# Performance work log

Measured on AMD Instinct MI355X. Metric: run time of the kernel, lower is better.

The kernel has to match this reference:

```python
import jax, jax.numpy as jnp
import numpy as np

# ---- constants from vecpar / module globals ----
N_SAMPLE = 500000
HID = 64       # shared_layers = [64]
HEAD = 32      # q*_layers width
PERIOD = 30
KAPPA, Y_BAR, B, C = 0.2, 2.0, 1.0, 0.1
GAMMA, RHO, SIGMA, DT = 1.2, 0.03, 0.03, 0.005


def _glorot(key, shape):
    fan_in, fan_out = shape
    std = (2.0 / (fan_in + fan_out)) ** 0.5
    return std * jax.random.normal(key, shape, dtype=jnp.float32)


def setup_inputs() -> dict:
    key = jax.random.key(0)
    ks = jax.random.split(key, 8)
    Y = jax.random.uniform(ks[0], (N_SAMPLE, 2), minval=0.05, maxval=5.0, dtype=jnp.float32)
    z = lambda n: jnp.zeros((n,), dtype=jnp.float32)
    return {
        'Y': Y,
        'W0': _glorot(ks[1], (2, HID)),   'b0': z(HID),
        'Wh1': _glorot(ks[2], (HID, HEAD)), 'bh1': z(HEAD), 'Wo1': _glorot(ks[3], (HEAD, 1)), 'bo1': z(1),
        'Wh2': _glorot(ks[4], (HID, HEAD)), 'bh2': z(HEAD), 'Wo2': _glorot(ks[5], (HEAD, 1)), 'bo2': z(1),
        'Wh3': _glorot(ks[6], (HID, HEAD)), 'bh3': z(HEAD), 'Wo3': _glorot(ks[7], (HEAD, 1)), 'bo3': z(1),
    }


def _net(Y2, Y3, W0, b0, Wh1, bh1, Wo1, bo1, Wh2, bh2, Wo2, bo2, Wh3, bh3, Wo3, bo3):
    # shared trunk: concat -> Dense(64) -> tanh; heads: Dense(32)->tanh->Dense(1)->exp
    h = jnp.tanh(jnp.concatenate([Y2, Y3], axis=1) @ W0 + b0)
    q1 = jnp.exp(jnp.tanh(h @ Wh1 + bh1) @ Wo1 + bo1)
    q2 = jnp.exp(jnp.tanh(h @ Wh2 + bh2) @ Wo2 + bo2)
    q3 = jnp.exp(jnp.tanh(h @ Wh3 + bh3) @ Wo3 + bo3)
    return q1, q2, q3


def _forward(Y, W0, b0, Wh1, bh1, Wo1, bo1, Wh2, bh2, Wo2, bo2, Wh3, bh3, Wo3, bo3):
    params = (W0, b0, Wh1, bh1, Wo1, bo1, Wh2, bh2, Wo2, bo2, Wh3, bh3, Wo3, bo3)
    f = lambda y2, y3: _net(y2, y3, *params)

    def q_and_grads(y2, y3):
        # per-row scalar sensitivities via two jvp passes (equiv. to tape.gradient)
        ones = jnp.ones_like(y2); zeros = jnp.zeros_like(y2)
        (q1, q2, q3), (d12, d22, d32) = jax.jvp(f, (y2, y3), (ones, zeros))
        _, (d13, d23, d33) = jax.jvp(f, (y2, y3), (zeros, ones))
        s11 = d12 * SIGMA / q1; s21 = d22 * SIGMA / q2; s31 = d32 * SIGMA / q3
        s12 = d13 * SIGMA / q1; s22 = d23 * SIGMA / q2; s32 = d33 * SIGMA / q3
        return (q1, q2, q3), (s11, s21, s31, s12, s22, s32)

    n = Y.shape[0]
    Y2 = Y[:, :1]; Y3 = Y[:, 1:2]
    (q1, q2, q3), (s11, s21, s31, s12, s22, s32) = q_and_grads(Y2, Y3)

    # dZ already scaled by sqrt(dt)
    noise = jnp.sqrt(jnp.asarray(DT, Y.dtype)) * jax.random.normal(
        jax.random.key(42), (PERIOD, n, 1, 2), dtype=Y.dtype)

    def step(carry, dZ):
        q1, q2, q3, Y2, Y3, s11, s21, s31, s12, s22, s32, loss = carry
        dZ1 = dZ[..., 0]; dZ2 = dZ[..., 1]
        W = q1 + q2 + q3
        q1h = q1 / W; q2h = q2 / W; q3h = 1 - q1h - q2h
        c = B * q1 - C * q1 ** 2 + Y2 + Y3
        sc1 = B * q1 * s11 - 2 * C * q1 ** 2 * s11 + SIGMA
        sc2 = B * q1 * s12 - 2 * C * q1 ** 2 * s12 + SIGMA
        sW1 = q1 * s11 + q2 * s21 + q3 * s31
        sW2 = q1 * s12 + q2 * s22 + q3 * s32
        g = GAMMA / (GAMMA - 1)
        sJ1 = g * (sc1 / c - sW1 / W); sJ2 = g * (sc2 / c - sW2 / W)
        p1 = (GAMMA * q1h * (s11 ** 2 + s12 ** 2)
              + GAMMA * q2h * (s11 * s21 + s12 * s22)
              + GAMMA * q3h * (s11 * s31 + s12 * s32)
              - (1 - GAMMA) * (sJ1 * s11 + sJ2 * s12))
        p2 = (GAMMA * q1h * (s11 * s21 + s12 * s22)
              + GAMMA * q2h * (s21 ** 2 + s22 ** 2)
              + GAMMA * q3h * (s21 * s31 + s22 * s32)
              - (1 - GAMMA) * (sJ1 * s21 + sJ2 * s22))
        p3 = (GAMMA * q1h * (s11 * s31 + s12 * s32)
              + GAMMA * q2h * (s21 * s31 + s22 * s32)
              + GAMMA * q3h * (s31 ** 2 + s32 ** 2)
              - (1 - GAMMA) * (sJ1 * s31 + sJ2 * s32))
        muY2 = KAPPA * (Y_BAR - Y2); muY3 = KAPPA * (Y_BAR - Y3)
        r = (RHO
             + GAMMA * ((B * q1 - 2 * C * q1 ** 2) * (p1 - (B - C * q1))
                        - C * q1 ** 2 * (s11 ** 2 + s12 ** 2) + muY2 + muY3) / c
             - GAMMA * (GAMMA + 1) / 2 * (sc1 ** 2 + sc2 ** 2) / c ** 2)
        r = r / (1 - GAMMA * (B * q1 - 2 * C * q1 ** 2) / c)
        mu1 = r + p1 - (B - C * q1)
        mu2 = r + p2 - Y2 / q2
        mu3 = r + p3 - Y3 / q3
        q1n = q1 * (1 + mu1 * DT + s11 * dZ1 + s12 * dZ2)
        q2n = q2 * (1 + mu2 * DT + s21 * dZ1 + s22 * dZ2)
        q3n = q3 * (1 + mu3 * DT + s31 * dZ1 + s32 * dZ2)
        Y2n = Y2 + muY2 * DT + SIGMA * dZ1
        Y3n = Y3 + muY3 * DT + SIGMA * dZ2
        (q1t, q2t, q3t), (ns11, ns21, ns31, ns12, ns22, ns32) = q_and_grads(Y2n, Y3n)
        loss = loss + jnp.sum((q1n - q1t) ** 2 + (q2n - q2t) ** 2 + (q3n - q3t) ** 2) / (n * PERIOD)
        return (q1n, q2n, q3n, Y2n, Y3n, ns11, ns21, ns31, ns12, ns22, ns32, loss), None

    init = (q1, q2, q3, Y2, Y3, s11, s21, s31, s12, s22, s32, jnp.asarray(0.0, Y.dtype))
    carry, _ = jax.lax.scan(step, init, noise)
    return carry[-1]


def reference(Y, W0, b0, Wh1, bh1, Wo1, bo1, Wh2, bh2, Wo2, bo2, Wh3, bh3, Wo3, bo3):
    return _forward(Y, W0, b0, Wh1, bh1, Wo1, bo1, Wh2, bh2, Wo2, bo2, Wh3, bh3, Wo3, bo3)
```

## Files before the change

kernel.cpp:

```cpp
#include <hip/hip_runtime.h>
#include <hip/hip_bf16.h>
#include <stdint.h>

#define NB 256
#define PERIOD 30

typedef __bf16  bf16x8 __attribute__((ext_vector_type(8)));
typedef float   f32x4  __attribute__((ext_vector_type(4)));
typedef float   f32x2  __attribute__((ext_vector_type(2)));
typedef unsigned int uint4v __attribute__((ext_vector_type(4)));

__device__ __forceinline__ float frcp(float x){ return __builtin_amdgcn_rcpf(x); }

__device__ __forceinline__ float fast_tanh(float x){
  float e = __expf(2.0f*x);
  return fmaf(-2.0f, frcp(e + 1.0f), 1.0f);
}

__device__ __forceinline__ unsigned int f2bfbits(float x){
  union { __hip_bfloat16 b; unsigned short u; } v;
  v.b = __float2bfloat16(x);
  return (unsigned int)v.u;
}
__device__ __forceinline__ unsigned int pack2bf(float lo, float hi){
  return f2bfbits(lo) | (f2bfbits(hi) << 16);
}

template <int CTRL>
__device__ __forceinline__ float dpp_add_step(float x){
  int y = __builtin_amdgcn_update_dpp(0, __float_as_int(x), CTRL, 0xf, 0xf, true);
  return x + __int_as_float(y);
}
__device__ __forceinline__ float row16_sum(float x){
  x = dpp_add_step<0xB1>(x);
  x = dpp_add_step<0x4E>(x);
  x = dpp_add_step<0x124>(x);
  x = dpp_add_step<0x128>(x);
  return x;
}

__device__ __forceinline__ void threefry2x32_k42(uint32_t x0, uint32_t x1,
                                                 uint32_t& o0, uint32_t& o1){
  const uint32_t ks0 = 0u, ks1 = 42u, ks2 = 0u ^ 42u ^ 0x1BD11BDAu;
  x0 += ks0; x1 += ks1;
#define TFR(rot) { x0 += x1; x1 = (x1 << (rot)) | (x1 >> (32 - (rot))); x1 ^= x0; }
  TFR(13) TFR(15) TFR(26) TFR(6)
  x0 += ks1; x1 += ks2 + 1u;
  TFR(17) TFR(29) TFR(16) TFR(24)
  x0 += ks2; x1 += ks0 + 2u;
  TFR(13) TFR(15) TFR(26) TFR(6)
  x0 += ks0; x1 += ks1 + 3u;
  TFR(17) TFR(29) TFR(16) TFR(24)
  x0 += ks1; x1 += ks2 + 4u;
  TFR(13) TFR(15) TFR(26) TFR(6)
  x0 += ks2; x1 += ks0 + 5u;
#undef TFR
  o0 = x0; o1 = x1;
}

__device__ __forceinline__ float normal_from_bits(uint32_t bits){
  float f = __uint_as_float((bits >> 9) | 0x3f800000u) - 1.0f;
  const float lo = -0.99999994f;
  float u = fmaf(f, 2.0f, lo);
  u = fmaxf(u, lo);
  float w = -log1pf(-u*u);
  float p;
  if (w < 5.0f){
    float ww = w - 2.5f;
    p = 2.81022636e-08f;
    p = fmaf(p, ww, 3.43273939e-07f);
    p = fmaf(p, ww, -3.5233877e-06f);
    p = fmaf(p, ww, -4.39150654e-06f);
    p = fmaf(p, ww, 0.00021858087f);
    p = fmaf(p, ww, -0.00125372503f);
    p = fmaf(p, ww, -0.00417768164f);
    p = fmaf(p, ww, 0.246640727f);
    p = fmaf(p, ww, 1.50140941f);
  } else {
    float ww = sqrtf(w) - 3.0f;
    p = -0.000200214257f;
    p = fmaf(p, ww, 0.000100950558f);
    p = fmaf(p, ww, 0.00134934322f);
    p = fmaf(p, ww, -0.00367342844f);
    p = fmaf(p, ww, 0.00573950773f);
    p = fmaf(p, ww, -0.0076224613f);
    p = fmaf(p, ww, 0.00943887047f);
    p = fmaf(p, ww, 1.00167406f);
    p = fmaf(p, ww, 2.83297682f);
  }
  return 1.41421356f * (p * u);
}

__device__ __forceinline__ void stage_tile(char* buf, int st, int grp, int colL,
    const unsigned int* hp, const unsigned int* up){
  if (grp == st){
    const int rbase = colL * 128;
    const int sw = (colL & 7) << 4;
#pragma unroll
    for (int w = 0; w < 8; ++w){
      int off = rbase + ((w * 16) ^ sw);
      *(uint4v*)(buf + off)        = uint4v{hp[w*4], hp[w*4+1], hp[w*4+2], hp[w*4+3]};
      *(uint4v*)(buf + 2048 + off) = uint4v{up[w*4], up[w*4+1], up[w*4+2], up[w*4+3]};
    }
  }
}

__device__ __forceinline__ void net_eval(
    float y2, float y3,
    const float* __restrict__ W0, const float* __restrict__ b0,
    char* sAw,
    const char* __restrict__ sBb,
    int colL, int grp,
    const float (&bh_v)[3][2], const float (&wo_v)[3][2], const float* bo_v,
    float& q1o, float& q2o, float& q3o,
    float& s11, float& s21, float& s31,
    float& s12, float& s22, float& s32)
{
  unsigned int hp[32], up[32];
#pragma unroll
  for (int d = 0; d < 32; ++d){
    f32x2 w0a = *(const f32x2*)(W0 + 2*d);
    f32x2 w0b = *(const f32x2*)(W0 + 64 + 2*d);
    f32x2 b0v = *(const f32x2*)(b0 + 2*d);
    f32x2 pre = y2 * w0a + (y3 * w0b + b0v);
    float hA = fast_tanh(pre.x), hB = fast_tanh(pre.y);
    f32x2 h  = {hA, hB};
    f32x2 u  = 1.0f - h * h;
    hp[d] = pack2bf(hA, hB);
    up[d] = pack2bf(u.x, u.y);
  }

  float qraw[3] = {0,0,0}, Araw[3] = {0,0,0}, Braw[3] = {0,0,0};
  const int bsw  = (colL & 7) << 4;
  const int srcL = ((colL >> 2) << 4) | colL;

#pragma unroll 1
  for (int st = 0; st < 4; ++st){
    stage_tile(sAw, st, grp, colL, hp, up);

    bf16x8 afh[2], afu[2];
#pragma unroll
    for (int kt = 0; kt < 2; ++kt){
      int off = colL*128 + ((kt*64 + grp*16) ^ bsw);
      afh[kt] = *(const bf16x8*)(sAw + off);
      afu[kt] = *(const bf16x8*)(sAw + 2048 + off);
    }

#pragma unroll
    for (int hd = 0; hd < 3; ++hd){
      f32x2 aq01 = {0,0}, aq23 = {0,0};
      f32x2 aA01 = {0,0}, aA23 = {0,0};
      f32x2 aB01 = {0,0}, aB23 = {0,0};
#pragma unroll
      for (int nt = 0; nt < 2; ++nt){
        bf16x8 bW[2], bA[2], bB[2];
#pragma unroll
        for (int kt = 0; kt < 2; ++kt){
          int rbase2 = (hd*96 + nt*16 + colL) * 128;
          int ko = ((kt*64 + grp*16) ^ bsw);
          bW[kt] = *(const bf16x8*)(sBb + rbase2 + ko);
          bA[kt] = *(const bf16x8*)(sBb + rbase2 + 4096 + ko);
          bB[kt] = *(const bf16x8*)(sBb + rbase2 + 8192 + ko);
        }
        f32x4 cAT = {0,0,0,0}, cA2 = {0,0,0,0}, cA3 = {0,0,0,0};
#pragma unroll
        for (int kt = 0; kt < 2; ++kt){
          cAT = __builtin_amdgcn_mfma_f32_16x16x32_bf16(afh[kt], bW[kt], cAT, 0, 0, 0);
          cA2 = __builtin_amdgcn_mfma_f32_16x16x32_bf16(afu[kt], bA[kt], cA2, 0, 0, 0);
          cA3 = __builtin_amdgcn_mfma_f32_16x16x32_bf16(afu[kt], bB[kt], cA3, 0, 0, 0);
        }
        float bh = bh_v[hd][nt], wo = wo_v[hd][nt];
        float t0 = fast_tanh(cAT[0] + bh);
        float t1 = fast_tanh(cAT[1] + bh);
        float t2 = fast_tanh(cAT[2] + bh);
        float t3 = fast_tanh(cAT[3] + bh);
        f32x2 dt01 = {fmaf(-t0, t0, 1.0f), fmaf(-t1, t1, 1.0f)};
        f32x2 dt23 = {fmaf(-t2, t2, 1.0f), fmaf(-t3, t3, 1.0f)};
        f32x2 wo2 = {wo, wo};
        aq01 = aq01 + f32x2{t0, t1} * wo2;
        aq23 = aq23 + f32x2{t2, t3} * wo2;
        aA01 = aA01 + dt01 * f32x2{cA2[0], cA2[1]};
        aA23 = aA23 + dt23 * f32x2{cA2[2], cA2[3]};
        aB01 = aB01 + dt01 * f32x2{cA3[0], cA3[1]};
        aB23 = aB23 + dt23 * f32x2{cA3[2], cA3[3]};
      }
      float rq0 = row16_sum(aq01.x), rq1 = row16_sum(aq01.y);
      float rq2 = row16_sum(aq23.x), rq3 = row16_sum(aq23.y);
      float rA0 = row16_sum(aA01.x), rA1 = row16_sum(aA01.y);
      float rA2 = row16_sum(aA23.x), rA3 = row16_sum(aA23.y);
      float rB0 = row16_sum(aB01.x), rB1 = row16_sum(aB01.y);
      float rB2 = row16_sum(aB23.x), rB3 = row16_sum(aB23.y);
      float qsel = (colL & 2) ? ((colL & 1) ? rq3 : rq2)
                              : ((colL & 1) ? rq1 : rq0);
      float asel = (colL & 2) ? ((colL & 1) ? rA3 : rA2)
                              : ((colL & 1) ? rA1 : rA0);
      float bsel = (colL & 2) ? ((colL & 1) ? rB3 : rB2)
                              : ((colL & 1) ? rB1 : rB0);
      float qp = __shfl(qsel, srcL, 64);
      float ap = __shfl(asel, srcL, 64);
      float bp = __shfl(bsel, srcL, 64);
      bool keep = (st == grp);
      qraw[hd] = keep ? qp : qraw[hd];
      Araw[hd] = keep ? ap : Araw[hd];
      Braw[hd] = keep ? bp : Braw[hd];
    }
  }

  q1o = __expf(qraw[0] + bo_v[0]);
  q2o = __expf(qraw[1] + bo_v[1]);
  q3o = __expf(qraw[2] + bo_v[2]);
  s11 = Araw[0]; s21 = Araw[1]; s31 = Araw[2];
  s12 = Braw[0]; s22 = Braw[1]; s32 = Braw[2];
}

__global__ __launch_bounds__(NB)
void sim_kernel(const float* __restrict__ Y,
  const float* __restrict__ W0,  const float* __restrict__ b0,
  const float* __restrict__ Wh1, const float* __restrict__ bh1,
  const float* __restrict__ Wo1, const float* __restrict__ bo1,
  const float* __restrict__ Wh2, const float* __restrict__ bh2,
  const float* __restrict__ Wo2, const float* __restrict__ bo2,
  const float* __restrict__ Wh3, const float* __restrict__ bh3,
  const float* __restrict__ Wo3, const float* __restrict__ bo3,
  float* __restrict__ out, int n)
{
  __shared__ __align__(16) char sB[288 * 128];
  __shared__ __align__(16) char sA[4][2 * 16 * 128];

  for (int e = threadIdx.x; e < 18432; e += NB){
    int hd   = e / 6144;
    int rem  = e - hd * 6144;
    int mat  = rem >> 11;
    int rem2 = rem & 2047;
    int j = rem2 >> 5, i = rem2 & 31;
    const float* W  = (hd == 0) ? Wh1 : (hd == 1) ? Wh2 : Wh3;
    const float* WO = (hd == 0) ? Wo1 : (hd == 1) ? Wo2 : Wo3;
    float wh = W[j * 32 + i];
    float sc = WO[i] * 0.03f;
    float v  = (mat == 0) ? wh
             : (mat == 1) ? W0[j] * wh * sc
                          : W0[64 + j] * wh * sc;
    int R   = hd * 96 + mat * 32 + i;
    int off = (R * 128 + j * 2) ^ ((R & 7) << 4);
    *(unsigned short*)(sB + off) = (unsigned short)f2bfbits(v);
  }
  __syncthreads();

  const int wv   = threadIdx.x >> 6;
  const int lane = threadIdx.x & 63;
  const int colL = lane & 15;
  const int grp  = lane >> 4;
  char* sAw = &sA[wv][0];

  float bh_v[3][2], wo_v[3][2], bo_v[3];
  {
    const float* BH[3] = {bh1, bh2, bh3};
    const float* WOp[3] = {Wo1, Wo2, Wo3};
#pragma unroll
    for (int hd = 0; hd < 3; ++hd)
#pragma unroll
      for (int nt = 0; nt < 2; ++nt){
        bh_v[hd][nt] = BH[hd][nt*16 + colL];
        wo_v[hd][nt] = WOp[hd][nt*16 + colL];
      }
    bo_v[0] = bo1[0]; bo_v[1] = bo2[0]; bo_v[2] = bo3[0];
  }

  const int gid = blockIdx.x * NB + threadIdx.x;
  const int ii  = (gid < n) ? gid : (n - 1);
  const float valid = (gid < n) ? 1.0f : 0.0f;

  const float2 yv = ((const float2*)Y)[ii];
  const float y2 = yv.x, y3 = yv.y;

  const float GAMMA = 1.2f, DT = 0.005f, SIGMA = 0.03f;
  const float KAPPA = 0.2f, YBAR = 2.0f, RHO = 0.03f, Bc = 1.0f, Cc = 0.1f;

  float q1,q2,q3,s11,s21,s31,s12,s22,s32;
  net_eval(y2, y3, W0, b0, sAw, sB, colL, grp, bh_v, wo_v, bo_v,
           q1,q2,q3,s11,s21,s31,s12,s22,s32);
  float Y2 = y2, Y3 = y3;
  float loss = 0.0f;

  for (int t = 0; t < PERIOD; ++t){
    uint32_t idx0 = 2u * ((uint32_t)t * (uint32_t)n + (uint32_t)ii);
    uint32_t a0, a1, c0, c1;
    threefry2x32_k42(0u, idx0,      a0, a1);
    threefry2x32_k42(0u, idx0 + 1u, c0, c1);
    float dZ1 = 0.070710678f * normal_from_bits(a0 ^ a1);
    float dZ2 = 0.070710678f * normal_from_bits(c0 ^ c1);

    float Wt  = q1 + q2 + q3;
    float q1h = q1 / Wt;
    float q2h = q2 / Wt;
    float q3h = 1.0f - q1h - q2h;
    float q1sq = q1 * q1;
    float c   = Bc*q1 - Cc*q1sq + Y2 + Y3;
    float bq  = Bc*q1 - 2.0f*Cc*q1sq;
    float sc1 = fmaf(bq, s11, SIGMA);
    float sc2 = fmaf(bq, s12, SIGMA);
    float sW1 = q1*s11 + q2*s21 + q3*s31;
    float sW2 = q1*s12 + q2*s22 + q3*s32;
    float sJ1 = 6.0f * (sc1/c - sW1/Wt);
    float sJ2 = 6.0f * (sc2/c - sW2/Wt);
    float d11 = s11*s11 + s12*s12;
    float d12 = s11*s21 + s12*s22;
    float d13 = s11*s31 + s12*s32;
    float d22 = s21*s21 + s22*s22;
    float d23 = s21*s31 + s22*s32;
    float d33 = s31*s31 + s32*s32;
    const float oneMG = 1.0f - GAMMA;
    float p1 = GAMMA*(q1h*d11 + q2h*d12 + q3h*d13) - oneMG*(sJ1*s11 + sJ2*s12);
    float p2 = GAMMA*(q1h*d12 + q2h*d22 + q3h*d23) - oneMG*(sJ1*s21 + sJ2*s22);
    float p3 = GAMMA*(q1h*d13 + q2h*d23 + q3h*d33) - oneMG*(sJ1*s31 + sJ2*s32);
    float muY2 = KAPPA * (YBAR - Y2);
    float muY3 = KAPPA * (YBAR - Y3);
    float r = RHO + GAMMA*(bq*(p1 - (Bc - Cc*q1)) - Cc*q1sq*d11 + muY2 + muY3)/c
                  - 1.32f*(sc1*sc1 + sc2*sc2)/(c*c);
    r = r / (1.0f - GAMMA*bq/c);
    float mu1 = r + p1 - (Bc - Cc*q1);
    float mu2 = r + p2 - Y2/q2;
    float mu3 = r + p3 - Y3/q3;
    float q1n = q1 * (1.0f + mu1*DT + s11*dZ1 + s12*dZ2);
    float q2n = q2 * (1.0f + mu2*DT + s21*dZ1 + s22*dZ2);
    float q3n = q3 * (1.0f + mu3*DT + s31*dZ1 + s32*dZ2);
    float Y2n = Y2 + muY2*DT + SIGMA*dZ1;
    float Y3n = Y3 + muY3*DT + SIGMA*dZ2;

    float qt1, qt2, qt3;
    net_eval(Y2n, Y3n, W0, b0, sAw, sB, colL, grp, bh_v, wo_v, bo_v,
             qt1,qt2,qt3, s11,s21,s31,s12,s22,s32);

    float e1 = q1n - qt1, e2 = q2n - qt2, e3 = q3n - qt3;
    loss += e1*e1 + e2*e2 + e3*e3;

    q1 = q1n; q2 = q2n; q3 = q3n; Y2 = Y2n; Y3 = Y3n;
  }

  loss *= valid * (1.0f / ((float)15000000));

#pragma unroll
  for (int off = 32; off > 0; off >>= 1)
    loss += __shfl_down(loss, off, 64);
  __shared__ float sred[NB / 64];
  if (lane == 0) sred[wv] = loss;
  __syncthreads();
  if (threadIdx.x == 0){
    float s = 0.0f;
#pragma unroll
    for (int w = 0; w < NB / 64; ++w) s += sred[w];
    atomicAdd(out, s);
  }
}

extern "C" void kernel_launch(void* const* d_in, const int* in_sizes, int n_in,
                              void* d_out, int out_size, void* d_ws, size_t ws_size,
                              hipStream_t stream)
{
  const float* Y   = (const float*)d_in[0];
  const float* W0  = (const float*)d_in[1];
  const float* b0  = (const float*)d_in[2];
  const float* Wh1 = (const float*)d_in[3];
  const float* bh1 = (const float*)d_in[4];
  const float* Wo1 = (const float*)d_in[5];
  const float* bo1 = (const float*)d_in[6];
  const float* Wh2 = (const float*)d_in[7];
  const float* bh2 = (const float*)d_in[8];
  const float* Wo2 = (const float*)d_in[9];
  const float* bo2 = (const float*)d_in[10];
  const float* Wh3 = (const float*)d_in[11];
  const float* bh3 = (const float*)d_in[12];
  const float* Wo3 = (const float*)d_in[13];
  const float* bo3 = (const float*)d_in[14];

  const int n = in_sizes[0] / 2;

  (void)hipMemsetAsync(d_out, 0, sizeof(float), stream);

  const int grid = (n + NB - 1) / NB;
  sim_kernel<<<grid, NB, 0, stream>>>(Y,
      W0, b0, Wh1, bh1, Wo1, bo1, Wh2, bh2, Wo2, bo2, Wh3, bh3, Wo3, bo3,
      (float*)d_out, n);
}
```

Measured before the change: 2.567 ms.

## Swap MFMA operands so hidden units land in rows, simplify reductions

The MFMA operands are transposed so each lane's four accumulator values run along the hidden dimension for a single sample column. The per-lane head reduction then becomes plain FMAs followed by two xor shuffles, replacing the 12 DPP row16 sums, the selects and the indexed shuffles. Head biases are folded into the MFMA accumulator init, and biases and output weights are read from shared memory as float4 instead of sitting in registers. The cost is extra LDS reads per tile in exchange for fewer cross-lane operations and lower register pressure.

```diff
diff --git a/kernel.cpp b/kernel.cpp
--- a/kernel.cpp
+++ b/kernel.cpp
@@ -24,19 +24,6 @@
 }
 __device__ __forceinline__ unsigned int pack2bf(float lo, float hi){
   return f2bfbits(lo) | (f2bfbits(hi) << 16);
-}
-
-template <int CTRL>
-__device__ __forceinline__ float dpp_add_step(float x){
-  int y = __builtin_amdgcn_update_dpp(0, __float_as_int(x), CTRL, 0xf, 0xf, true);
-  return x + __int_as_float(y);
-}
-__device__ __forceinline__ float row16_sum(float x){
-  x = dpp_add_step<0xB1>(x);
-  x = dpp_add_step<0x4E>(x);
-  x = dpp_add_step<0x124>(x);
-  x = dpp_add_step<0x128>(x);
-  return x;
 }
 
 __device__ __forceinline__ void threefry2x32_k42(uint32_t x0, uint32_t x1,
@@ -110,8 +97,10 @@
     const float* __restrict__ W0, const float* __restrict__ b0,
     char* sAw,
     const char* __restrict__ sBb,
+    const float* __restrict__ sBH,
+    const float* __restrict__ sWO,
     int colL, int grp,
-    const float (&bh_v)[3][2], const float (&wo_v)[3][2], const float* bo_v,
+    const float* bo_v,
     float& q1o, float& q2o, float& q3o,
     float& s11, float& s21, float& s31,
     float& s12, float& s22, float& s32)
@@ -131,8 +120,7 @@
   }
 
   float qraw[3] = {0,0,0}, Araw[3] = {0,0,0}, Braw[3] = {0,0,0};
-  const int bsw  = (colL & 7) << 4;
-  const int srcL = ((colL >> 2) << 4) | colL;
+  const int bsw = (colL & 7) << 4;
 
 #pragma unroll 1
   for (int st = 0; st < 4; ++st){
@@ -148,9 +136,7 @@
 
 #pragma unroll
     for (int hd = 0; hd < 3; ++hd){
-      f32x2 aq01 = {0,0}, aq23 = {0,0};
-      f32x2 aA01 = {0,0}, aA23 = {0,0};
-      f32x2 aB01 = {0,0}, aB23 = {0,0};
+      float aq = 0.0f, aA = 0.0f, aB = 0.0f;
 #pragma unroll
       for (int nt = 0; nt < 2; ++nt){
         bf16x8 bW[2], bA[2], bB[2];
@@ -162,47 +148,44 @@
           bA[kt] = *(const bf16x8*)(sBb + rbase2 + 4096 + ko);
           bB[kt] = *(const bf16x8*)(sBb + rbase2 + 8192 + ko);
         }
-        f32x4 cAT = {0,0,0,0}, cA2 = {0,0,0,0}, cA3 = {0,0,0,0};
+        f32x4 bh4 = *(const f32x4*)(sBH + hd*32 + nt*16 + grp*4);
+        f32x4 wo4 = *(const f32x4*)(sWO + hd*32 + nt*16 + grp*4);
+        f32x4 cAT = bh4;
+        f32x4 cA2 = {0,0,0,0}, cA3 = {0,0,0,0};
 #pragma unroll
         for (int kt = 0; kt < 2; ++kt){
-          cAT = __builtin_amdgcn_mfma_f32_16x16x32_bf16(afh[kt], bW[kt], cAT, 0, 0, 0);
-          cA2 = __builtin_amdgcn_mfma_f32_16x16x32_bf16(afu[kt], bA[kt], cA2, 0, 0, 0);
-          cA3 = __builtin_amdgcn_mfma_f32_16x16x32_bf16(afu[kt], bB[kt], cA3, 0, 0, 0);
+          cAT = __builtin_amdgcn_mfma_f32_16x16x32_bf16(bW[kt], afh[kt], cAT, 0, 0, 0);
+          cA2 = __builtin_amdgcn_mfma_f32_16x16x32_bf16(bA[kt], afu[kt], cA2, 0, 0, 0);
+          cA3 = __builtin_amdgcn_mfma_f32_16x16x32_bf16(bB[kt], afu[kt], cA3, 0, 0, 0);
         }
-        float bh = bh_v[hd][nt], wo = wo_v[hd][nt];
-        float t0 = fast_tanh(cAT[0] + bh);
-        float t1 = fast_tanh(cAT[1] + bh);
-        float t2 = fast_tanh(cAT[2] + bh);
-        float t3 = fast_tanh(cAT[3] + bh);
-        f32x2 dt01 = {fmaf(-t0, t0, 1.0f), fmaf(-t1, t1, 1.0f)};
-        f32x2 dt23 = {fmaf(-t2, t2, 1.0f), fmaf(-t3, t3, 1.0f)};
-        f32x2 wo2 = {wo, wo};
-        aq01 = aq01 + f32x2{t0, t1} * wo2;
-        aq23 = aq23 + f32x2{t2, t3} * wo2;
-        aA01 = aA01 + dt01 * f32x2{cA2[0], cA2[1]};
-        aA23 = aA23 + dt23 * f32x2{cA2[2], cA2[3]};
-        aB01 = aB01 + dt01 * f32x2{cA3[0], cA3[1]};
-        aB23 = aB23 + dt23 * f32x2{cA3[2], cA3[3]};
+        float t0 = fast_tanh(cAT[0]);
+        float t1 = fast_tanh(cAT[1]);
+        float t2 = fast_tanh(cAT[2]);
+        float t3 = fast_tanh(cAT[3]);
+        aq = fmaf(t0, wo4[0], aq);
+        aq = fmaf(t1, wo4[1], aq);
+        aq = fmaf(t2, wo4[2], aq);
+        aq = fmaf(t3, wo4[3], aq);
+        float dt0 = fmaf(-t0, t0, 1.0f);
+        float dt1 = fmaf(-t1, t1, 1.0f);
+        float dt2 = fmaf(-t2, t2, 1.0f);
+        float dt3 = fmaf(-t3, t3, 1.0f);
+        aA = fmaf(dt0, cA2[0], aA);
+        aA = fmaf(dt1, cA2[1], aA);
+        aA = fmaf(dt2, cA2[2], aA);
+        aA = fmaf(dt3, cA2[3], aA);
+        aB = fmaf(dt0, cA3[0], aB);
+        aB = fmaf(dt1, cA3[1], aB);
+        aB = fmaf(dt2, cA3[2], aB);
+        aB = fmaf(dt3, cA3[3], aB);
       }
-      float rq0 = row16_sum(aq01.x), rq1 = row16_sum(aq01.y);
-      float rq2 = row16_sum(aq23.x), rq3 = row16_sum(aq23.y);
-      float rA0 = row16_sum(aA01.x), rA1 = row16_sum(aA01.y);
-      float rA2 = row16_sum(aA23.x), rA3 = row16_sum(aA23.y);
-      float rB0 = row16_sum(aB01.x), rB1 = row16_sum(aB01.y);
-      float rB2 = row16_sum(aB23.x), rB3 = row16_sum(aB23.y);
-      float qsel = (colL & 2) ? ((colL & 1) ? rq3 : rq2)
-                              : ((colL & 1) ? rq1 : rq0);
-      float asel = (colL & 2) ? ((colL & 1) ? rA3 : rA2)
-                              : ((colL & 1) ? rA1 : rA0);
-      float bsel = (colL & 2) ? ((colL & 1) ? rB3 : rB2)
-                              : ((colL & 1) ? rB1 : rB0);
-      float qp = __shfl(qsel, srcL, 64);
-      float ap = __shfl(asel, srcL, 64);
-      float bp = __shfl(bsel, srcL, 64);
+      aq += __shfl_xor(aq, 16, 64);  aq += __shfl_xor(aq, 32, 64);
+      aA += __shfl_xor(aA, 16, 64);  aA += __shfl_xor(aA, 32, 64);
+      aB += __shfl_xor(aB, 16, 64);  aB += __shfl_xor(aB, 32, 64);
       bool keep = (st == grp);
-      qraw[hd] = keep ? qp : qraw[hd];
-      Araw[hd] = keep ? ap : Araw[hd];
-      Braw[hd] = keep ? bp : Braw[hd];
+      qraw[hd] = keep ? aq : qraw[hd];
+      Araw[hd] = keep ? aA : Araw[hd];
+      Braw[hd] = keep ? aB : Braw[hd];
     }
   }
 
@@ -226,6 +209,8 @@
 {
   __shared__ __align__(16) char sB[288 * 128];
   __shared__ __align__(16) char sA[4][2 * 16 * 128];
+  __shared__ __align__(16) float sBH[96];
+  __shared__ __align__(16) float sWO[96];
 
   for (int e = threadIdx.x; e < 18432; e += NB){
     int hd   = e / 6144;
@@ -244,6 +229,13 @@
     int off = (R * 128 + j * 2) ^ ((R & 7) << 4);
     *(unsigned short*)(sB + off) = (unsigned short)f2bfbits(v);
   }
+  if (threadIdx.x < 96){
+    int hd = threadIdx.x >> 5, row = threadIdx.x & 31;
+    const float* BH = (hd == 0) ? bh1 : (hd == 1) ? bh2 : bh3;
+    const float* WO = (hd == 0) ? Wo1 : (hd == 1) ? Wo2 : Wo3;
+    sBH[threadIdx.x] = BH[row];
+    sWO[threadIdx.x] = WO[row];
+  }
   __syncthreads();
 
   const int wv   = threadIdx.x >> 6;
@@ -252,19 +244,7 @@
   const int grp  = lane >> 4;
   char* sAw = &sA[wv][0];
 
-  float bh_v[3][2], wo_v[3][2], bo_v[3];
-  {
-    const float* BH[3] = {bh1, bh2, bh3};
-    const float* WOp[3] = {Wo1, Wo2, Wo3};
-#pragma unroll
-    for (int hd = 0; hd < 3; ++hd)
-#pragma unroll
-      for (int nt = 0; nt < 2; ++nt){
-        bh_v[hd][nt] = BH[hd][nt*16 + colL];
-        wo_v[hd][nt] = WOp[hd][nt*16 + colL];
-      }
-    bo_v[0] = bo1[0]; bo_v[1] = bo2[0]; bo_v[2] = bo3[0];
-  }
+  float bo_v[3] = {bo1[0], bo2[0], bo3[0]};
 
   const int gid = blockIdx.x * NB + threadIdx.x;
   const int ii  = (gid < n) ? gid : (n - 1);
@@ -277,7 +257,7 @@
   const float KAPPA = 0.2f, YBAR = 2.0f, RHO = 0.03f, Bc = 1.0f, Cc = 0.1f;
 
   float q1,q2,q3,s11,s21,s31,s12,s22,s32;
-  net_eval(y2, y3, W0, b0, sAw, sB, colL, grp, bh_v, wo_v, bo_v,
+  net_eval(y2, y3, W0, b0, sAw, sB, sBH, sWO, colL, grp, bo_v,
            q1,q2,q3,s11,s21,s31,s12,s22,s32);
   float Y2 = y2, Y3 = y3;
   float loss = 0.0f;
@@ -328,7 +308,7 @@
     float Y3n = Y3 + muY3*DT + SIGMA*dZ2;
 
     float qt1, qt2, qt3;
-    net_eval(Y2n, Y3n, W0, b0, sAw, sB, colL, grp, bh_v, wo_v, bo_v,
+    net_eval(Y2n, Y3n, W0, b0, sAw, sB, sBH, sWO, colL, grp, bo_v,
              qt1,qt2,qt3, s11,s21,s31,s12,s22,s32);
 
     float e1 = q1n - qt1, e2 = q2n - qt2, e3 = q3n - qt3;
```

Result: faster. 2.207 ms, median of 2 (-14.0%).
